# Kernel optimization log

Hardware: AMD Instinct MI355X
Metric: run time of the kernel (lower is better)

The kernel has to match this reference:

```python
import jax, jax.numpy as jnp
import numpy as np

BS, SL, D_IN, D_MODEL, H = 4, 128, 512, 512, 8
DP = D_MODEL // H


def setup_inputs() -> dict:
    key = jax.random.key(0)
    ks = jax.random.split(key, 12)
    s = 0.02
    inp = {
        "q": jax.random.normal(ks[0], (BS, SL, D_IN), jnp.float32),
        "k": jax.random.normal(ks[1], (BS, SL, D_IN), jnp.float32),
        "v": jax.random.normal(ks[2], (BS, SL, D_IN), jnp.float32),
    }
    j = jnp.arange(SL)
    # mask[t, jk] = 1.0 for the zero-padded slots jk > t in the shuffled sequence for step t
    mask2d = (j[None, :] > j[:, None]).astype(jnp.float32)  # (SL, SL)
    inp["mask"] = mask2d[None, :, None, None, :]            # (1, SL, 1, 1, SL)
    for i, n in enumerate(["wq", "wk", "wv", "dense"]):
        din = D_IN if n != "dense" else D_MODEL
        inp[n + "_w"] = jax.random.normal(ks[3 + 2 * i], (din, D_MODEL), jnp.float32) * s
        inp[n + "_b"] = jnp.zeros((D_MODEL,), jnp.float32)
    return inp


def _shuffle_idx(key, sl):
    # Row t of returned idx: random permutation of [0..t-1], then t, then t+1.. (padding slots).
    u = jax.random.uniform(key, (sl, sl))
    j = jnp.arange(sl)
    t = j[:, None]
    sort_keys = jnp.where(j[None, :] < t, u, j[None, :].astype(jnp.float32) + 2.0)
    return jnp.argsort(sort_keys, axis=-1)  # (sl, sl) int32


def _split_heads_shuffled(x, idx, valid):
    # x: (bs, sl, d) -> (bs, sl, H, sl, DP); padding slots (j > t) zeroed like torch plc_holder
    bs, sl, d = x.shape
    xt = x[:, idx, :] * valid[None, :, :, None]  # (bs, sl, sl, d)
    xt = xt.reshape(bs, sl, sl, H, DP)
    return xt.transpose(0, 1, 3, 2, 4)


def reference(q, k, v, mask, wq_w, wq_b, wk_w, wk_b, wv_w, wv_b, dense_w, dense_b):
    bs, sl, _ = q.shape
    j = jnp.arange(sl)
    valid = (j[None, :] <= j[:, None]).astype(q.dtype)  # (sl, sl)
    pkey = jax.random.key(42)
    idx_q = _shuffle_idx(jax.random.fold_in(pkey, 0), sl)
    idx_k = _shuffle_idx(jax.random.fold_in(pkey, 1), sl)
    idx_v = _shuffle_idx(jax.random.fold_in(pkey, 2), sl)

    qp = q @ wq_w + wq_b
    kp = k @ wk_w + wk_b
    vp = v @ wv_w + wv_b

    qh = _split_heads_shuffled(qp, idx_q, valid)  # (bs, sl, H, sl, DP)
    kh = _split_heads_shuffled(kp, idx_k, valid)
    vh = _split_heads_shuffled(vp, idx_v, valid)

    logits = jnp.einsum('bthqd,bthkd->bthqk', qh, kh) / jnp.sqrt(jnp.float32(DP))
    logits = logits + mask * (-1e9)
    attn = jax.nn.softmax(logits, axis=-1)          # (bs, sl, H, sl, sl)
    ctx = jnp.einsum('bthqk,bthkd->bthqd', attn, vh)  # (bs, sl, H, sl, DP)

    ctx = ctx.transpose(0, 1, 3, 2, 4).reshape(bs, sl, sl, H * DP)
    eff = ctx[:, j, j, :]                           # query row t of step t (the token itself)
    out = eff @ dense_w + dense_b                   # (bs, sl, d_model); dropout p=0 -> identity
    return (out, attn)
```

## Files before the change

kernel.cpp:

```cpp
#include <hip/hip_runtime.h>
#include <stdint.h>


#define BSZ 4
#define SLEN 128
#define DMODEL 512
#define NHEAD 8
#define HDIM 64

__device__ __forceinline__ uint32_t rotl32(uint32_t v, int d) {
  return (v << d) | (v >> (32 - d));
}

__device__ __forceinline__ void tf2x32(uint32_t k0, uint32_t k1, uint32_t x0,
                                       uint32_t x1, uint32_t& y0, uint32_t& y1) {
  uint32_t ks2 = k0 ^ k1 ^ 0x1BD11BDAu;
  x0 += k0; x1 += k1;
#define TF_R(r) { x0 += x1; x1 = rotl32(x1, (r)); x1 ^= x0; }
  TF_R(13) TF_R(15) TF_R(26) TF_R(6)
  x0 += k1;  x1 += ks2 + 1u;
  TF_R(17) TF_R(29) TF_R(16) TF_R(24)
  x0 += ks2; x1 += k0 + 2u;
  TF_R(13) TF_R(15) TF_R(26) TF_R(6)
  x0 += k0;  x1 += k1 + 3u;
  TF_R(17) TF_R(29) TF_R(16) TF_R(24)
  x0 += k1;  x1 += ks2 + 4u;
  TF_R(13) TF_R(15) TF_R(26) TF_R(6)
  x0 += ks2; x1 += k0 + 5u;
#undef TF_R
  y0 = x0; y1 = x1;
}

__device__ __forceinline__ uint16_t f32_to_bf16(float v) {
  uint32_t x = __float_as_uint(v);
  return (uint16_t)((x + 0x7FFFu + ((x >> 16) & 1u)) >> 16);
}
__device__ __forceinline__ float bf16_to_f32(uint16_t b) {
  return __uint_as_float(((uint32_t)b) << 16);
}

__global__ __launch_bounds__(128) void idx_kernel(int* __restrict__ idx) {
  const int m = blockIdx.x;
  const int t = blockIdx.y;
  const int j = threadIdx.x;
  __shared__ float u[SLEN];
  uint32_t fk0, fk1;
  tf2x32(0u, 42u, 0u, (uint32_t)m, fk0, fk1);
  const int flat = t * SLEN + j;
  uint32_t y0, y1;
  tf2x32(fk0, fk1, 0u, (uint32_t)flat, y0, y1);
  uint32_t bits = y0 ^ y1;
  float uu = __uint_as_float((bits >> 9) | 0x3f800000u) - 1.0f;
  u[j] = uu;
  __syncthreads();
  int* row = idx + (m * SLEN + t) * SLEN;
  if (j >= t) {
    row[j] = j;
  } else {
    int rank = 0;
    for (int i = 0; i < t; ++i) {
      float ui = u[i];
      rank += ((ui < uu) || (ui == uu && i < j)) ? 1 : 0;
    }
    row[rank] = j;
  }
}

__device__ __forceinline__ void gemm512_body(const float* __restrict__ A,
                                             const float* __restrict__ W,
                                             const float* __restrict__ bias,
                                             float* __restrict__ C,
                                             float* As , float* Ws ) {
  const int tid = threadIdx.x;
  const int tx = tid & 15, ty = tid >> 4;
  const int row0 = blockIdx.y * 64, col0 = blockIdx.x * 64;
  const int lr = tid >> 2, lc = (tid & 3) << 2;
  const int wr = tid >> 4, wc = (tid & 15) << 2;
  float acc[4][4] = {};
  for (int k0 = 0; k0 < 512; k0 += 16) {
    float4 av = *(const float4*)(A + (size_t)(row0 + lr) * 512 + k0 + lc);
    float4 wv = *(const float4*)(W + (size_t)(k0 + wr) * 512 + col0 + wc);
    As[lr * 17 + lc + 0] = av.x; As[lr * 17 + lc + 1] = av.y;
    As[lr * 17 + lc + 2] = av.z; As[lr * 17 + lc + 3] = av.w;
    *(float4*)(Ws + wr * 64 + wc) = wv;
    __syncthreads();
#pragma unroll
    for (int kk = 0; kk < 16; ++kk) {
      float a[4], b[4];
#pragma unroll
      for (int i = 0; i < 4; ++i) a[i] = As[(ty * 4 + i) * 17 + kk];
#pragma unroll
      for (int jj = 0; jj < 4; ++jj) b[jj] = Ws[kk * 64 + tx * 4 + jj];
#pragma unroll
      for (int i = 0; i < 4; ++i)
#pragma unroll
        for (int jj = 0; jj < 4; ++jj) acc[i][jj] += a[i] * b[jj];
    }
    __syncthreads();
  }
#pragma unroll
  for (int i = 0; i < 4; ++i) {
    int r = row0 + ty * 4 + i, c = col0 + tx * 4;
    float4 o;
    o.x = acc[i][0] + bias[c + 0];
    o.y = acc[i][1] + bias[c + 1];
    o.z = acc[i][2] + bias[c + 2];
    o.w = acc[i][3] + bias[c + 3];
    *(float4*)(C + (size_t)r * 512 + c) = o;
  }
}

__global__ __launch_bounds__(256) void proj_kernel(
    const float* __restrict__ q, const float* __restrict__ k, const float* __restrict__ v,
    const float* __restrict__ wq, const float* __restrict__ wk, const float* __restrict__ wv,
    const float* __restrict__ bq, const float* __restrict__ bk, const float* __restrict__ bv,
    float* __restrict__ qp, float* __restrict__ kp, float* __restrict__ vp) {
  __shared__ float As[64 * 17];
  __shared__ float Ws[16 * 64];
  const float* A; const float* W; const float* B; float* C;
  if (blockIdx.z == 0)      { A = q; W = wq; B = bq; C = qp; }
  else if (blockIdx.z == 1) { A = k; W = wk; B = bk; C = kp; }
  else                      { A = v; W = wv; B = bv; C = vp; }
  gemm512_body(A, W, B, C, As, Ws);
}

__global__ __launch_bounds__(256) void dense_kernel(const float* __restrict__ A,
                                                    const float* __restrict__ W,
                                                    const float* __restrict__ B,
                                                    float* __restrict__ C) {
  __shared__ float As[64 * 17];
  __shared__ float Ws[16 * 64];
  gemm512_body(A, W, B, C, As, Ws);
}

__global__ __launch_bounds__(256) void sef_kernel(const float* __restrict__ qp,
                                                  const float* __restrict__ kp,
                                                  uint16_t* __restrict__ E,
                                                  float* __restrict__ Ft) {
  const int h = blockIdx.x, b = blockIdx.y;
  const int tid = threadIdx.x;
  __shared__ float qs[32 * 132];
  __shared__ float ks[32 * 132];
  __shared__ float redm[128 * 16];
  __shared__ float csum[128 * 16];
  __shared__ float m127s[SLEN];
  const float* qbase = qp + ((size_t)b * SLEN) * DMODEL + h * HDIM;
  const float* kbase = kp + ((size_t)b * SLEN) * DMODEL + h * HDIM;
  const int i0 = (tid >> 4) * 8, jg = tid & 15, j0 = jg * 8;
  float acc[8][8] = {};
  for (int d0 = 0; d0 < HDIM; d0 += 32) {
    __syncthreads();
    for (int it = 0; it < 4; ++it) {
      int flat = it * 256 + tid;
      int row = flat >> 3;
      int c4 = (flat & 7) << 2;
      float4 a = *(const float4*)(qbase + (size_t)row * DMODEL + d0 + c4);
      float4 bb = *(const float4*)(kbase + (size_t)row * DMODEL + d0 + c4);
      qs[(c4 + 0) * 132 + row] = a.x;  qs[(c4 + 1) * 132 + row] = a.y;
      qs[(c4 + 2) * 132 + row] = a.z;  qs[(c4 + 3) * 132 + row] = a.w;
      ks[(c4 + 0) * 132 + row] = bb.x; ks[(c4 + 1) * 132 + row] = bb.y;
      ks[(c4 + 2) * 132 + row] = bb.z; ks[(c4 + 3) * 132 + row] = bb.w;
    }
    __syncthreads();
    for (int d = 0; d < 32; ++d) {
      float4 qa = *(const float4*)(qs + d * 132 + i0);
      float4 qb = *(const float4*)(qs + d * 132 + i0 + 4);
      float4 ka = *(const float4*)(ks + d * 132 + j0);
      float4 kb = *(const float4*)(ks + d * 132 + j0 + 4);
      float a[8] = {qa.x, qa.y, qa.z, qa.w, qb.x, qb.y, qb.z, qb.w};
      float bb[8] = {ka.x, ka.y, ka.z, ka.w, kb.x, kb.y, kb.z, kb.w};
#pragma unroll
      for (int r = 0; r < 8; ++r)
#pragma unroll
        for (int c = 0; c < 8; ++c) acc[r][c] += a[r] * bb[c];
    }
  }
#pragma unroll
  for (int r = 0; r < 8; ++r) {
    float m = -3.402823466e38f;
#pragma unroll
    for (int c = 0; c < 8; ++c) {
      acc[r][c] *= 0.125f;
      m = fmaxf(m, acc[r][c]);
    }
    redm[(i0 + r) * 16 + jg] = m;
  }
  __syncthreads();
  if (tid < SLEN) {
    float m = redm[tid * 16];
#pragma unroll
    for (int g = 1; g < 16; ++g) m = fmaxf(m, redm[tid * 16 + g]);
    m127s[tid] = m;
  }
  __syncthreads();
  const int bh = b * NHEAD + h;
  uint16_t* Eb = E + (size_t)bh * SLEN * SLEN;
#pragma unroll
  for (int r = 0; r < 8; ++r) {
    const float m = m127s[i0 + r];
    float run = 0.f;
    ushort4 e0, e1;
    float ev;
    ev = __expf(acc[r][0] - m); e0.x = f32_to_bf16(ev); run += ev; acc[r][0] = run;
    ev = __expf(acc[r][1] - m); e0.y = f32_to_bf16(ev); run += ev; acc[r][1] = run;
    ev = __expf(acc[r][2] - m); e0.z = f32_to_bf16(ev); run += ev; acc[r][2] = run;
    ev = __expf(acc[r][3] - m); e0.w = f32_to_bf16(ev); run += ev; acc[r][3] = run;
    ev = __expf(acc[r][4] - m); e1.x = f32_to_bf16(ev); run += ev; acc[r][4] = run;
    ev = __expf(acc[r][5] - m); e1.y = f32_to_bf16(ev); run += ev; acc[r][5] = run;
    ev = __expf(acc[r][6] - m); e1.z = f32_to_bf16(ev); run += ev; acc[r][6] = run;
    ev = __expf(acc[r][7] - m); e1.w = f32_to_bf16(ev); run += ev; acc[r][7] = run;
    *(ushort4*)(Eb + (size_t)(i0 + r) * SLEN + j0) = e0;
    *(ushort4*)(Eb + (size_t)(i0 + r) * SLEN + j0 + 4) = e1;
    csum[(i0 + r) * 16 + jg] = run;
  }
  __syncthreads();
  float* Fb = Ft + (size_t)bh * SLEN * SLEN;
#pragma unroll
  for (int r = 0; r < 8; ++r) {
    float base = 0.f;
    for (int g = 0; g < 16; ++g) {
      if (g == jg) break;
      base += csum[(i0 + r) * 16 + g];
    }
#pragma unroll
    for (int c = 0; c < 8; ++c)
      Fb[(size_t)(j0 + c) * SLEN + (i0 + r)] = 1.0f / (base + acc[r][c]);
  }
}

__global__ __launch_bounds__(256) void attn_kernel(const uint16_t* __restrict__ E,
                                                   const float* __restrict__ Ft,
                                                   const int* __restrict__ idx,
                                                   const float* __restrict__ vp,
                                                   float* __restrict__ attn_out,
                                                   float* __restrict__ eff) {
  const int h = blockIdx.x, t = blockIdx.y, b = blockIdx.z;
  const int tid = threadIdx.x;
  const int wave = tid >> 6, lane = tid & 63;
  const int half = lane >> 5;
  const int l32 = lane & 31;
  __shared__ int iqs[SLEN], iks[SLEN], ivs[SLEN];
  __shared__ float Fs[SLEN];
  __shared__ float arow[SLEN];
  __shared__ float red[256];
  const int bh = b * NHEAD + h;
  if (tid < SLEN) {
    iqs[tid] = idx[(0 * SLEN + t) * SLEN + tid];
    iks[tid] = idx[(1 * SLEN + t) * SLEN + tid];
    ivs[tid] = idx[(2 * SLEN + t) * SLEN + tid];
    Fs[tid] = Ft[((size_t)bh * SLEN + t) * SLEN + tid];
  }
  __syncthreads();
  const uint16_t* Eb = E + (size_t)bh * SLEN * SLEN;
  const float inv = 1.0f / (float)(t + 1);
  float* obase = attn_out + ((size_t)((b * SLEN + t) * NHEAD + h)) * SLEN * SLEN;
  const int k0 = l32 * 4;
  const int ikA = iks[k0], ikB = iks[k0 + 1], ikC = iks[k0 + 2], ikD = iks[k0 + 3];
  float4 cm;
  cm.x = (k0 + 0 <= t) ? 1.f : 0.f;
  cm.y = (k0 + 1 <= t) ? 1.f : 0.f;
  cm.z = (k0 + 2 <= t) ? 1.f : 0.f;
  cm.w = (k0 + 3 <= t) ? 1.f : 0.f;
#pragma unroll 2
  for (int q8 = wave * 2; q8 < SLEN; q8 += 8) {
    const int qe = q8 + half;
    float4 val;
    if (qe <= t) {
      const int iq = iqs[qe];
      const float f = Fs[iq];
      const uint16_t* Er = Eb + (size_t)iq * SLEN;
      val.x = bf16_to_f32(Er[ikA]) * f * cm.x;
      val.y = bf16_to_f32(Er[ikB]) * f * cm.y;
      val.z = bf16_to_f32(Er[ikC]) * f * cm.z;
      val.w = bf16_to_f32(Er[ikD]) * f * cm.w;
    } else {
      val.x = inv * cm.x; val.y = inv * cm.y;
      val.z = inv * cm.z; val.w = inv * cm.w;
    }
    *(float4*)(obase + (size_t)qe * SLEN + k0) = val;
    if (qe == t) *(float4*)(arow + k0) = val;
  }
  __syncthreads();
  {
    const int d = tid & 63, kg = tid >> 6;
    const float* vb = vp + (size_t)b * SLEN * DMODEL + h * HDIM + d;
    float acc = 0.f;
    for (int k = kg; k <= t; k += 4) acc += arow[k] * vb[(size_t)ivs[k] * DMODEL];
    red[tid] = acc;
  }
  __syncthreads();
  if (tid < HDIM) {
    eff[((size_t)b * SLEN + t) * DMODEL + h * HDIM + tid] =
        red[tid] + red[tid + 64] + red[tid + 128] + red[tid + 192];
  }
}

extern "C" void kernel_launch(void* const* d_in, const int* in_sizes, int n_in,
                              void* d_out, int out_size, void* d_ws, size_t ws_size,
                              hipStream_t stream) {
  const float* q    = (const float*)d_in[0];
  const float* k    = (const float*)d_in[1];
  const float* v    = (const float*)d_in[2];
  const float* wq_w = (const float*)d_in[4];
  const float* wq_b = (const float*)d_in[5];
  const float* wk_w = (const float*)d_in[6];
  const float* wk_b = (const float*)d_in[7];
  const float* wv_w = (const float*)d_in[8];
  const float* wv_b = (const float*)d_in[9];
  const float* dw   = (const float*)d_in[10];
  const float* db   = (const float*)d_in[11];

  float* out  = (float*)d_out;
  float* attn = out + 262144;

  float* wsf = (float*)d_ws;
  uint16_t* E = (uint16_t*)wsf;
  int*   idx = (int*)(wsf + 262144);
  float* qp  = wsf + 311296;
  float* kp  = qp + 262144;
  float* vp  = kp + 262144;
  float* Ft  = vp + 262144;
  float* eff = Ft + 524288;
  (void)in_sizes; (void)n_in; (void)out_size; (void)ws_size;

  idx_kernel<<<dim3(3, 128, 1), 128, 0, stream>>>(idx);
  proj_kernel<<<dim3(8, 8, 3), 256, 0, stream>>>(q, k, v, wq_w, wk_w, wv_w,
                                                 wq_b, wk_b, wv_b, qp, kp, vp);
  sef_kernel<<<dim3(8, 4, 1), 256, 0, stream>>>(qp, kp, E, Ft);
  attn_kernel<<<dim3(8, 128, 4), 256, 0, stream>>>(E, Ft, idx, vp, attn, eff);
  dense_kernel<<<dim3(8, 8, 1), 256, 0, stream>>>(eff, dw, db, out);
}
```

Measured before the change: 407.4 us.

## Stage E tile in LDS and process eight timesteps per attention block

Each attention block now copies the whole 128x128 bf16 score tile for its (batch, head) into shared memory and handles eight consecutive timesteps instead of one, so the gathered E reads hit LDS rather than global memory. The context row is recomputed directly from E and F, with a wave-shuffle reduction, instead of going through an arow buffer and extra block barriers. The grid shrinks eightfold (512 blocks) and shared-memory use rises to about 48 KB, which lowers occupancy and parallelism. The kernel is likely bound by the attn output write, so gains may be limited.

Measured after the change: 421.5 us. +3.5%, slower.

```diff
diff --git a/kernel.cpp b/kernel.cpp
--- a/kernel.cpp
+++ b/kernel.cpp
@@ -234,64 +234,80 @@
                                                    const float* __restrict__ vp,
                                                    float* __restrict__ attn_out,
                                                    float* __restrict__ eff) {
-  const int h = blockIdx.x, t = blockIdx.y, b = blockIdx.z;
+  const int h = blockIdx.x;
+  const int tg = blockIdx.y;
+  const int b = blockIdx.z;
   const int tid = threadIdx.x;
   const int wave = tid >> 6, lane = tid & 63;
-  const int half = lane >> 5;
-  const int l32 = lane & 31;
-  __shared__ int iqs[SLEN], iks[SLEN], ivs[SLEN];
-  __shared__ float Fs[SLEN];
-  __shared__ float arow[SLEN];
-  __shared__ float red[256];
+  const int half = lane >> 5, l32 = lane & 31;
   const int bh = b * NHEAD + h;
-  if (tid < SLEN) {
-    iqs[tid] = idx[(0 * SLEN + t) * SLEN + tid];
-    iks[tid] = idx[(1 * SLEN + t) * SLEN + tid];
-    ivs[tid] = idx[(2 * SLEN + t) * SLEN + tid];
-    Fs[tid] = Ft[((size_t)bh * SLEN + t) * SLEN + tid];
-  }
-  __syncthreads();
-  const uint16_t* Eb = E + (size_t)bh * SLEN * SLEN;
-  const float inv = 1.0f / (float)(t + 1);
-  float* obase = attn_out + ((size_t)((b * SLEN + t) * NHEAD + h)) * SLEN * SLEN;
+  __shared__ __align__(16) uint16_t Es[SLEN * SLEN];
+  __shared__ int iqs[8][SLEN];
+  __shared__ int iks[8][SLEN];
+  __shared__ int ivs[8][SLEN];
+  __shared__ float Fsl[8][SLEN];
+  {
+    const uint4* src = (const uint4*)(E + (size_t)bh * SLEN * SLEN);
+    uint4* dst = (uint4*)Es;
+#pragma unroll
+    for (int i = 0; i < 8; ++i) dst[i * 256 + tid] = src[i * 256 + tid];
+  }
+  {
+    const int t0 = tg * 8;
+#pragma unroll
+    for (int ii = 0; ii < 4; ++ii) {
+      int i = ii * 256 + tid;
+      int s = i >> 7, j = i & 127;
+      int t = t0 + s;
+      iqs[s][j] = idx[(0 * SLEN + t) * SLEN + j];
+      iks[s][j] = idx[(1 * SLEN + t) * SLEN + j];
+      ivs[s][j] = idx[(2 * SLEN + t) * SLEN + j];
+      Fsl[s][j] = Ft[((size_t)bh * SLEN + t) * SLEN + j];
+    }
+  }
+  __syncthreads();
   const int k0 = l32 * 4;
-  const int ikA = iks[k0], ikB = iks[k0 + 1], ikC = iks[k0 + 2], ikD = iks[k0 + 3];
-  float4 cm;
-  cm.x = (k0 + 0 <= t) ? 1.f : 0.f;
-  cm.y = (k0 + 1 <= t) ? 1.f : 0.f;
-  cm.z = (k0 + 2 <= t) ? 1.f : 0.f;
-  cm.w = (k0 + 3 <= t) ? 1.f : 0.f;
+  const int d = (wave << 4) + (lane >> 2);
+  const int kg = lane & 3;
+  const float* vb = vp + (size_t)b * SLEN * DMODEL + h * HDIM + d;
+  for (int s = 0; s < 8; ++s) {
+    const int t = tg * 8 + s;
+    const int ikA = iks[s][k0], ikB = iks[s][k0 + 1], ikC = iks[s][k0 + 2], ikD = iks[s][k0 + 3];
+    float4 cm;
+    cm.x = (k0 + 0 <= t) ? 1.f : 0.f;
+    cm.y = (k0 + 1 <= t) ? 1.f : 0.f;
+    cm.z = (k0 + 2 <= t) ? 1.f : 0.f;
+    cm.w = (k0 + 3 <= t) ? 1.f : 0.f;
+    const float inv = 1.0f / (float)(t + 1);
+    float* obase = attn_out + ((size_t)((b * SLEN + t) * NHEAD + h)) * SLEN * SLEN;
 #pragma unroll 2
-  for (int q8 = wave * 2; q8 < SLEN; q8 += 8) {
-    const int qe = q8 + half;
-    float4 val;
-    if (qe <= t) {
-      const int iq = iqs[qe];
-      const float f = Fs[iq];
-      const uint16_t* Er = Eb + (size_t)iq * SLEN;
-      val.x = bf16_to_f32(Er[ikA]) * f * cm.x;
-      val.y = bf16_to_f32(Er[ikB]) * f * cm.y;
-      val.z = bf16_to_f32(Er[ikC]) * f * cm.z;
-      val.w = bf16_to_f32(Er[ikD]) * f * cm.w;
-    } else {
-      val.x = inv * cm.x; val.y = inv * cm.y;
-      val.z = inv * cm.z; val.w = inv * cm.w;
-    }
-    *(float4*)(obase + (size_t)qe * SLEN + k0) = val;
-    if (qe == t) *(float4*)(arow + k0) = val;
-  }
-  __syncthreads();
-  {
-    const int d = tid & 63, kg = tid >> 6;
-    const float* vb = vp + (size_t)b * SLEN * DMODEL + h * HDIM + d;
-    float acc = 0.f;
-    for (int k = kg; k <= t; k += 4) acc += arow[k] * vb[(size_t)ivs[k] * DMODEL];
-    red[tid] = acc;
-  }
-  __syncthreads();
-  if (tid < HDIM) {
-    eff[((size_t)b * SLEN + t) * DMODEL + h * HDIM + tid] =
-        red[tid] + red[tid + 64] + red[tid + 128] + red[tid + 192];
+    for (int q8 = wave * 2; q8 < SLEN; q8 += 8) {
+      const int qe = q8 + half;
+      float4 val;
+      if (qe <= t) {
+        const int iq = iqs[s][qe];
+        const float f = Fsl[s][iq];
+        const uint16_t* Er = Es + iq * SLEN;
+        val.x = bf16_to_f32(Er[ikA]) * f * cm.x;
+        val.y = bf16_to_f32(Er[ikB]) * f * cm.y;
+        val.z = bf16_to_f32(Er[ikC]) * f * cm.z;
+        val.w = bf16_to_f32(Er[ikD]) * f * cm.w;
+      } else {
+        val.x = inv * cm.x; val.y = inv * cm.y;
+        val.z = inv * cm.z; val.w = inv * cm.w;
+      }
+      *(float4*)(obase + (size_t)qe * SLEN + k0) = val;
+    }
+    {
+      const uint16_t* Et = Es + t * SLEN;
+      float acc = 0.f;
+      for (int k = kg; k <= t; k += 4)
+        acc += bf16_to_f32(Et[iks[s][k]]) * vb[(size_t)ivs[s][k] * DMODEL];
+      acc += __shfl_xor(acc, 1);
+      acc += __shfl_xor(acc, 2);
+      if (kg == 0)
+        eff[((size_t)b * SLEN + t) * DMODEL + h * HDIM + d] = acc * Fsl[s][t];
+    }
   }
 }
 
@@ -327,6 +343,6 @@
   proj_kernel<<<dim3(8, 8, 3), 256, 0, stream>>>(q, k, v, wq_w, wk_w, wv_w,
                                                  wq_b, wk_b, wv_b, qp, kp, vp);
   sef_kernel<<<dim3(8, 4, 1), 256, 0, stream>>>(qp, kp, E, Ft);
-  attn_kernel<<<dim3(8, 128, 4), 256, 0, stream>>>(E, Ft, idx, vp, attn, eff);
+  attn_kernel<<<dim3(8, 16, 4), 256, 0, stream>>>(E, Ft, idx, vp, attn, eff);
   dense_kernel<<<dim3(8, 8, 1), 256, 0, stream>>>(eff, dw, db, out);
 }
```
